# Performance work log

Hardware: AMD Instinct MI355X
Metric: run time of the kernel (lower is better)

The kernel has to match this reference:

```python
import jax, jax.numpy as jnp
import numpy as np

B, S, E, H, O = 4, 2048, 1024, 8, 128

def setup_inputs() -> dict:
    key = jax.random.key(0)
    k1, k2, k3, k4, k5 = jax.random.split(key, 5)
    return {
        "x":  jax.random.normal(k1, (B, S, E), dtype=jnp.float32),
        "Wq": jax.random.normal(k2, (H, E, O), dtype=jnp.float32),
        "Wk": jax.random.normal(k3, (E, O), dtype=jnp.float32),
        "Wv": jax.random.normal(k4, (E, O), dtype=jnp.float32),
        "Wo": jax.random.normal(k5, (O * H, E), dtype=jnp.float32),
    }

def reference(x, Wq, Wk, Wv, Wo):
    # self-attention: kv = x; mode='multihead' (no causal mask), attn_mask=None
    Q = jnp.einsum('bse,heo->bhso', x, Wq)        # (B,H,S,O) per-head query proj
    K = x @ Wk                                     # (B,S,O) shared across heads
    V = x @ Wv                                     # (B,S,O)
    scale = 1.0 / jnp.sqrt(jnp.float32(O))
    scores = jnp.einsum('bhqo,bko->bhqk', Q, K) * scale  # (B,H,S,S)
    probs = jax.nn.softmax(scores, axis=-1)
    ctx = jnp.einsum('bhqk,bko->bhqo', probs, V)   # (B,H,S,O)
    ctx = ctx.transpose(0, 2, 1, 3).reshape(B, S, H * O)  # (B,S,H*O)
    return ctx @ Wo                                # (B,S,E)
```

## Files before the change

kernel.cpp:

```cpp
#include <hip/hip_runtime.h>
#include <math.h>


typedef __attribute__((ext_vector_type(8))) short bf16x8;
typedef __attribute__((ext_vector_type(4))) float f32x4;

#define MFMA(a, b, c) __builtin_amdgcn_mfma_f32_16x16x32_bf16((a), (b), (c), 0, 0, 0)
#define GLB(p) ((const __attribute__((address_space(1))) void*)(p))
#define LDS(p) ((__attribute__((address_space(3))) void*)(p))

#if __has_builtin(__builtin_amdgcn_exp2f)
#define EXP2F(x) __builtin_amdgcn_exp2f(x)
#else
#define EXP2F(x) exp2f(x)
#endif

__device__ __forceinline__ short f2bf(float f) {
    union { float f; unsigned u; } v; v.f = f;
    unsigned r = v.u + 0x7fffu + ((v.u >> 16) & 1u);
    return (short)(r >> 16);
}
__device__ __forceinline__ float bf2f(short s) {
    union { unsigned u; float f; } v; v.u = ((unsigned)(unsigned short)s) << 16;
    return v.f;
}


__global__ __launch_bounds__(256) void split_kernel(
    const float* __restrict__ x, short* __restrict__ hi, short* __restrict__ lo, int n) {
    for (int i = blockIdx.x * blockDim.x + threadIdx.x; i < n; i += gridDim.x * blockDim.x) {
        float f = x[i];
        short h = f2bf(f);
        hi[i] = h;
        lo[i] = f2bf(f - bf2f(h));
    }
}

__global__ __launch_bounds__(256) void build_wt(
    const float* __restrict__ Wq, const float* __restrict__ Wk, const float* __restrict__ Wv,
    short* __restrict__ wth, short* __restrict__ wtl) {
    const int total = 1280 * 1024;
    for (int idx = blockIdx.x * blockDim.x + threadIdx.x; idx < total; idx += gridDim.x * blockDim.x) {
        int n = idx >> 10, k = idx & 1023;
        float f;
        if (n < 1024)      f = Wq[((size_t)(n >> 7) * 1024 + k) * 128 + (n & 127)];
        else if (n < 1152) f = Wk[(size_t)k * 128 + (n - 1024)];
        else               f = Wv[(size_t)k * 128 + (n - 1152)];
        short h = f2bf(f);
        wth[idx] = h;
        wtl[idx] = f2bf(f - bf2f(h));
    }
}

__global__ __launch_bounds__(256) void build_wot(
    const float* __restrict__ Wo, short* __restrict__ wot) {
    const int total = 1024 * 1024;
    for (int idx = blockIdx.x * blockDim.x + threadIdx.x; idx < total; idx += gridDim.x * blockDim.x) {
        int e = idx >> 10, k = idx & 1023;
        wot[idx] = f2bf(Wo[(size_t)k * 1024 + e]);
    }
}

template <int MODE>
__global__ __launch_bounds__(256, 4) void gemm_k(
    const short* __restrict__ Ah, const short* __restrict__ Al,
    const short* __restrict__ Bth, const short* __restrict__ Btl,
    short* __restrict__ qh, short* __restrict__ ql,
    short* __restrict__ kh, short* __restrict__ kl,
    short* __restrict__ vt, float* __restrict__ outf) {
    constexpr int K = 1024;
    __shared__ __align__(16) char smem[33792];
    short* As_h = (short*)smem;
    short* Bs_h = (short*)(smem + 8192);
    short* As_l = (short*)(smem + 16384);
    short* Bs_l = (short*)(smem + 24576);
    unsigned* Ep = (unsigned*)smem;

    const int t = threadIdx.x;
    const int m0 = blockIdx.x * 128, n0 = blockIdx.y * 128;
    const int wave = t >> 6, lane = t & 63;
    const int wr = wave >> 1, wc = wave & 1;
    const int quad = lane >> 4, l16 = lane & 15;
    const bool needLo = (MODE == 0) && (blockIdx.y < 9);

    f32x4 acc[4][4];
    for (int i = 0; i < 4; ++i)
        for (int j = 0; j < 4; ++j) acc[i][j] = (f32x4){0.f, 0.f, 0.f, 0.f};

    for (int kb = 0; kb < K / 32; ++kb) {
        __syncthreads();
        for (int i = 0; i < 2; ++i) {
            int slot = (wave * 2 + i) * 64 + lane;
            int row = slot >> 2, ch = slot & 3;
            int ldsoff = (wave * 2 + i) * 512;
            size_t ga = (size_t)(m0 + row) * K + kb * 32 + ch * 8;
            size_t gb = (size_t)(n0 + row) * K + kb * 32 + ch * 8;
            __builtin_amdgcn_global_load_lds(GLB(Ah + ga), LDS(&As_h[ldsoff]), 16, 0, 0);
            __builtin_amdgcn_global_load_lds(GLB(Bth + gb), LDS(&Bs_h[ldsoff]), 16, 0, 0);
            if constexpr (MODE == 0) {
                if (needLo) {
                    __builtin_amdgcn_global_load_lds(GLB(Al + ga), LDS(&As_l[ldsoff]), 16, 0, 0);
                    __builtin_amdgcn_global_load_lds(GLB(Btl + gb), LDS(&Bs_l[ldsoff]), 16, 0, 0);
                }
            }
        }
        __syncthreads();

        bf16x8 a[4], b[4];
        for (int mi = 0; mi < 4; ++mi)
            a[mi] = *(const bf16x8*)&As_h[(wr * 64 + mi * 16 + l16) * 32 + quad * 8];
        for (int ni = 0; ni < 4; ++ni)
            b[ni] = *(const bf16x8*)&Bs_h[(wc * 64 + ni * 16 + l16) * 32 + quad * 8];
        for (int mi = 0; mi < 4; ++mi)
            for (int ni = 0; ni < 4; ++ni)
                acc[mi][ni] = MFMA(a[mi], b[ni], acc[mi][ni]);
        if constexpr (MODE == 0) {
            if (needLo) {
                bf16x8 al[4], bl[4];
                for (int mi = 0; mi < 4; ++mi)
                    al[mi] = *(const bf16x8*)&As_l[(wr * 64 + mi * 16 + l16) * 32 + quad * 8];
                for (int ni = 0; ni < 4; ++ni)
                    bl[ni] = *(const bf16x8*)&Bs_l[(wc * 64 + ni * 16 + l16) * 32 + quad * 8];
                for (int mi = 0; mi < 4; ++mi)
                    for (int ni = 0; ni < 4; ++ni) {
                        acc[mi][ni] = MFMA(a[mi], bl[ni], acc[mi][ni]);
                        acc[mi][ni] = MFMA(al[mi], b[ni], acc[mi][ni]);
                    }
            }
        }
    }

    const float qscale = 0.12753102455195157f;
    for (int p = 0; p < 2; ++p) {
        __syncthreads();
        if (wr == p) {
            for (int mi = 0; mi < 4; ++mi) {
                int rl = mi * 16 + quad * 4;
                for (int ni = 0; ni < 4; ++ni) {
                    int cl = wc * 64 + ni * 16 + l16;
                    for (int r = 0; r < 4; ++r) {
                        float v = acc[mi][ni][r];
                        unsigned pk;
                        if constexpr (MODE == 0) {
                            if (blockIdx.y < 8) v *= qscale;
                            short hv = f2bf(v);
                            short lv = f2bf(v - bf2f(hv));
                            pk = (unsigned)(unsigned short)hv |
                                 ((unsigned)(unsigned short)lv << 16);
                        } else {
                            union { float f; unsigned u; } cv; cv.f = v; pk = cv.u;
                        }
                        Ep[(rl + r) * 132 + cl] = pk;
                    }
                }
            }
        }
        __syncthreads();

        if constexpr (MODE == 1) {
            for (int j = 0; j < 8; ++j) {
                int cid = t + j * 256;
                int row = cid >> 5, c = cid & 31;
                f32x4 val;
                for (int q = 0; q < 4; ++q) {
                    union { unsigned u; float f; } cv;
                    cv.u = Ep[row * 132 + c * 4 + q];
                    val[q] = cv.f;
                }
                int gr = m0 + p * 64 + row;
                *(f32x4*)&outf[(size_t)gr * 1024 + n0 + c * 4] = val;
            }
        } else if (blockIdx.y < 9) {
            for (int j = 0; j < 4; ++j) {
                int cid = t + j * 256;
                int row = cid >> 4, c = cid & 15;
                bf16x8 hv, lv;
                for (int q = 0; q < 8; ++q) {
                    unsigned w = Ep[row * 132 + c * 8 + q];
                    hv[q] = (short)(w & 0xffffu);
                    lv[q] = (short)(w >> 16);
                }
                int gr = m0 + p * 64 + row;
                int bb = gr >> 11, s = gr & 2047;
                if (blockIdx.y < 8) {
                    size_t base = (((size_t)(bb * 8 + (n0 >> 7))) * 2048 + s) * 128 + c * 8;
                    *(bf16x8*)&qh[base] = hv;
                    *(bf16x8*)&ql[base] = lv;
                } else {
                    size_t base = ((size_t)bb * 2048 + s) * 128 + c * 8;
                    *(bf16x8*)&kh[base] = hv;
                    *(bf16x8*)&kl[base] = lv;
                }
            }
        } else {
            for (int j = 0; j < 4; ++j) {
                int cid = t + j * 256;
                int d = cid >> 3, sc = cid & 7;
                bf16x8 hv;
                for (int q = 0; q < 8; ++q) {
                    unsigned w = Ep[(sc * 8 + q) * 132 + d];
                    hv[q] = (short)(w & 0xffffu);
                }
                int gr0 = m0 + p * 64 + sc * 8;
                int bb = gr0 >> 11, s0 = gr0 & 2047;
                *(bf16x8*)&vt[((size_t)bb * 128 + d) * 2048 + s0] = hv;
            }
        }
    }
}

__global__ __launch_bounds__(256, 2) void attn_k(
    const short* __restrict__ qh, const short* __restrict__ ql,
    const short* __restrict__ kh, const short* __restrict__ kl,
    const short* __restrict__ vt, short* __restrict__ ctx) {
    constexpr int S = 2048, D = 128;
    __shared__ short Kh_s[64 * 128];
    __shared__ short Kl_s[64 * 128];
    __shared__ short Vt_s[128 * 64];
    __shared__ short P_s[128 * 72];

    const int bh = blockIdx.y, b = bh >> 3, h = bh & 7;
    const int q0 = blockIdx.x * 128;
    const int t = threadIdx.x, wave = t >> 6, lane = t & 63;
    const int quad = lane >> 4, l16 = lane & 15;
    const int e8 = l16 & 7;

    bf16x8 bones;
    {
        short o = (l16 == 0) ? (short)0x3F80 : (short)0;
        for (int j = 0; j < 8; ++j) bones[j] = o;
    }

    bf16x8 qfh[2][4], qfl[2][4];
    for (int mb = 0; mb < 2; ++mb) {
        size_t qbase = ((size_t)(b * 8 + h) * S + q0 + wave * 32 + mb * 16 + l16) * D + quad * 8;
        for (int c = 0; c < 4; ++c) {
            qfh[mb][c] = *(const bf16x8*)(qh + qbase + c * 32);
            qfl[mb][c] = *(const bf16x8*)(ql + qbase + c * 32);
        }
    }

    float mrow[2][4];
    f32x4 oacc[2][8], lacc[2];
    for (int mb = 0; mb < 2; ++mb) {
        for (int r = 0; r < 4; ++r) mrow[mb][r] = -INFINITY;
        for (int oi = 0; oi < 8; ++oi) oacc[mb][oi] = (f32x4){0.f, 0.f, 0.f, 0.f};
        lacc[mb] = (f32x4){0.f, 0.f, 0.f, 0.f};
    }

    if (((blockIdx.x + (blockIdx.y << 4)) >> 8) & 1) {
        for (int i = 0; i < 13; ++i) __builtin_amdgcn_s_sleep(7);
    }

    for (int kt = 0; kt < S / 64; ++kt) {
        __syncthreads();
        {
            int pch = lane & 15;
            for (int i = 0; i < 4; ++i) {
                int rk = wave * 16 + i * 4 + (lane >> 4);
                int j = pch ^ (rk & 7);
                size_t g = ((size_t)b * S + kt * 64 + rk) * D + j * 8;
                int ldsoff = (wave * 16 + i * 4) * 128;
                __builtin_amdgcn_global_load_lds(GLB(kh + g), LDS(&Kh_s[ldsoff]), 16, 0, 0);
                __builtin_amdgcn_global_load_lds(GLB(kl + g), LDS(&Kl_s[ldsoff]), 16, 0, 0);
            }
        }
        {
            int pch = lane & 7;
            for (int i = 0; i < 4; ++i) {
                int rv = wave * 32 + i * 8 + (lane >> 3);
                int j = pch ^ (rv & 7);
                size_t g = ((size_t)b * D + rv) * S + kt * 64 + j * 8;
                int ldsoff = (wave * 32 + i * 8) * 64;
                __builtin_amdgcn_global_load_lds(GLB(vt + g), LDS(&Vt_s[ldsoff]), 16, 0, 0);
            }
        }
        __syncthreads();

        f32x4 sacc[2][4];
        for (int mb = 0; mb < 2; ++mb)
            for (int ni = 0; ni < 4; ++ni) sacc[mb][ni] = (f32x4){0.f, 0.f, 0.f, 0.f};
        for (int ni = 0; ni < 4; ++ni) {
            for (int c = 0; c < 4; ++c) {
                int off = (ni * 16 + l16) * 128 + ((c * 4 + quad) ^ e8) * 8;
                bf16x8 kbh = *(const bf16x8*)&Kh_s[off];
                bf16x8 kbl = *(const bf16x8*)&Kl_s[off];
                __builtin_amdgcn_s_setprio(1);
                for (int mb = 0; mb < 2; ++mb) {
                    sacc[mb][ni] = MFMA(qfh[mb][c], kbh, sacc[mb][ni]);
                    sacc[mb][ni] = MFMA(qfl[mb][c], kbh, sacc[mb][ni]);
                    sacc[mb][ni] = MFMA(qfh[mb][c], kbl, sacc[mb][ni]);
                }
                __builtin_amdgcn_s_setprio(0);
            }
        }

        for (int mb = 0; mb < 2; ++mb) {
            for (int r = 0; r < 4; ++r) {
                float mx = fmaxf(fmaxf(sacc[mb][0][r], sacc[mb][1][r]),
                                 fmaxf(sacc[mb][2][r], sacc[mb][3][r]));
                for (int off = 8; off; off >>= 1) mx = fmaxf(mx, __shfl_xor(mx, off));
                float mnew = fmaxf(mrow[mb][r], mx);
                float alpha = EXP2F(mrow[mb][r] - mnew);
                mrow[mb][r] = mnew;
                for (int ni = 0; ni < 4; ++ni)
                    sacc[mb][ni][r] = EXP2F(sacc[mb][ni][r] - mnew);
                lacc[mb][r] *= alpha;
                for (int oi = 0; oi < 8; ++oi) oacc[mb][oi][r] *= alpha;
            }
            for (int ni = 0; ni < 4; ++ni)
                for (int r = 0; r < 4; ++r) {
                    union { float f; unsigned u; } cv; cv.f = sacc[mb][ni][r];
                    P_s[(wave * 32 + mb * 16 + quad * 4 + r) * 72 + ni * 16 + l16] =
                        (short)((cv.u + 0x8000u) >> 16);
                }
        }

        for (int c2 = 0; c2 < 2; ++c2) {
            bf16x8 pa[2];
            for (int mb = 0; mb < 2; ++mb) {
                pa[mb] = *(const bf16x8*)&P_s[(wave * 32 + mb * 16 + l16) * 72 + c2 * 32 + quad * 8];
                lacc[mb] = MFMA(pa[mb], bones, lacc[mb]);
            }
            for (int oi = 0; oi < 8; ++oi) {
                int off = (oi * 16 + l16) * 64 + ((c2 * 4 + quad) ^ e8) * 8;
                bf16x8 vb = *(const bf16x8*)&Vt_s[off];
                __builtin_amdgcn_s_setprio(1);
                for (int mb = 0; mb < 2; ++mb)
                    oacc[mb][oi] = MFMA(pa[mb], vb, oacc[mb][oi]);
                __builtin_amdgcn_s_setprio(0);
            }
        }
    }

    for (int mb = 0; mb < 2; ++mb) {
        for (int r = 0; r < 4; ++r) {
            float ls = __shfl(lacc[mb][r], lane & 48);
            float inv = 1.f / ls;
            int s = q0 + wave * 32 + mb * 16 + quad * 4 + r;
            size_t base = ((size_t)b * S + s) * 1024 + h * 128;
            for (int oi = 0; oi < 8; ++oi)
                ctx[base + oi * 16 + l16] = f2bf(oacc[mb][oi][r] * inv);
        }
    }
}


extern "C" void kernel_launch(void* const* d_in, const int* in_sizes, int n_in,
                              void* d_out, int out_size, void* d_ws, size_t ws_size,
                              hipStream_t stream) {
    const float* x  = (const float*)d_in[0];
    const float* Wq = (const float*)d_in[1];
    const float* Wk = (const float*)d_in[2];
    const float* Wv = (const float*)d_in[3];
    const float* Wo = (const float*)d_in[4];
    float* out = (float*)d_out;

    char* p = (char*)d_ws;
    auto alloc = [&](size_t bytes) { char* r = p; p += bytes; return r; };
    short* xh  = (short*)alloc(16777216);
    short* xl  = (short*)alloc(16777216);
    short* wth = (short*)alloc(2621440);
    short* wtl = (short*)alloc(2621440);
    short* wot = (short*)alloc(2097152);
    short* qh  = (short*)alloc(16777216);
    short* ql  = (short*)alloc(16777216);
    short* kh  = (short*)alloc(2097152);
    short* kl  = (short*)alloc(2097152);
    short* vt  = (short*)alloc(2097152);
    short* ctx = (short*)alloc(16777216);

    split_kernel<<<dim3(2048), dim3(256), 0, stream>>>(x, xh, xl, 8192 * 1024);
    build_wt<<<dim3(1280), dim3(256), 0, stream>>>(Wq, Wk, Wv, wth, wtl);
    build_wot<<<dim3(1024), dim3(256), 0, stream>>>(Wo, wot);
    gemm_k<0><<<dim3(64, 10), dim3(256), 0, stream>>>(xh, xl, wth, wtl,
                                                      qh, ql, kh, kl, vt, nullptr);
    attn_k<<<dim3(16, 32), dim3(256), 0, stream>>>(qh, ql, kh, kl, vt, ctx);
    gemm_k<1><<<dim3(64, 8), dim3(256), 0, stream>>>(ctx, nullptr, wot, nullptr,
                                                     nullptr, nullptr, nullptr, nullptr,
                                                     nullptr, out);
}
```

Before: 359.0 us.

## Vectorize input split, tile-transpose weight prep, drop attention stagger sleep

The fp32-to-bf16 hi/lo split of x now loads four floats at a time and stores packed 4-short vectors. The weight transposes for Wq/Wk/Wv and Wo go through a padded 32x32 shared-memory tile, so both reads and writes are coalesced instead of strided gathers. The s_sleep stagger that delayed half the attention blocks is removed. Together these target memory inefficiency in the preprocessing kernels and idle time in attention, though dropping the stagger may change cache or bandwidth contention patterns.

```diff
diff --git a/kernel.cpp b/kernel.cpp
--- a/kernel.cpp
+++ b/kernel.cpp
@@ -4,6 +4,7 @@
 
 typedef __attribute__((ext_vector_type(8))) short bf16x8;
 typedef __attribute__((ext_vector_type(4))) float f32x4;
+typedef __attribute__((ext_vector_type(4))) short s16x4;
 
 #define MFMA(a, b, c) __builtin_amdgcn_mfma_f32_16x16x32_bf16((a), (b), (c), 0, 0, 0)
 #define GLB(p) ((const __attribute__((address_space(1))) void*)(p))
@@ -27,37 +28,73 @@
 
 
 __global__ __launch_bounds__(256) void split_kernel(
-    const float* __restrict__ x, short* __restrict__ hi, short* __restrict__ lo, int n) {
-    for (int i = blockIdx.x * blockDim.x + threadIdx.x; i < n; i += gridDim.x * blockDim.x) {
-        float f = x[i];
-        short h = f2bf(f);
-        hi[i] = h;
-        lo[i] = f2bf(f - bf2f(h));
+    const float* __restrict__ x, short* __restrict__ hi, short* __restrict__ lo, int n4) {
+    for (int i = blockIdx.x * blockDim.x + threadIdx.x; i < n4; i += gridDim.x * blockDim.x) {
+        f32x4 v = *(const f32x4*)&x[(size_t)i * 4];
+        s16x4 h, l;
+        for (int j = 0; j < 4; ++j) {
+            float f = v[j];
+            short hh = f2bf(f);
+            h[j] = hh;
+            l[j] = f2bf(f - bf2f(hh));
+        }
+        *(s16x4*)&hi[(size_t)i * 4] = h;
+        *(s16x4*)&lo[(size_t)i * 4] = l;
     }
 }
 
 __global__ __launch_bounds__(256) void build_wt(
     const float* __restrict__ Wq, const float* __restrict__ Wk, const float* __restrict__ Wv,
     short* __restrict__ wth, short* __restrict__ wtl) {
-    const int total = 1280 * 1024;
-    for (int idx = blockIdx.x * blockDim.x + threadIdx.x; idx < total; idx += gridDim.x * blockDim.x) {
-        int n = idx >> 10, k = idx & 1023;
-        float f;
-        if (n < 1024)      f = Wq[((size_t)(n >> 7) * 1024 + k) * 128 + (n & 127)];
-        else if (n < 1152) f = Wk[(size_t)k * 128 + (n - 1024)];
-        else               f = Wv[(size_t)k * 128 + (n - 1152)];
-        short h = f2bf(f);
-        wth[idx] = h;
-        wtl[idx] = f2bf(f - bf2f(h));
+    __shared__ float tile[32][33];
+    const int m = blockIdx.z;
+    const int k0 = blockIdx.x * 32, o0 = blockIdx.y * 32;
+    const float* src = (m < 8) ? (Wq + (size_t)m * 1024 * 128) : (m == 8 ? Wk : Wv);
+    const int base_n = (m < 8) ? m * 128 : (m == 8 ? 1024 : 1152);
+    const int t = threadIdx.x;
+    {
+        int tx = t & 31, ty = t >> 5;
+        for (int p = 0; p < 4; ++p)
+            tile[ty + p * 8][tx] = src[(size_t)(k0 + ty + p * 8) * 128 + o0 + tx];
+    }
+    __syncthreads();
+    {
+        int kx = (t & 15) * 2, oy = t >> 4;
+        for (int p = 0; p < 2; ++p) {
+            int o = oy + p * 16;
+            float f0 = tile[kx][o], f1 = tile[kx + 1][o];
+            short h0 = f2bf(f0), h1 = f2bf(f1);
+            short l0 = f2bf(f0 - bf2f(h0)), l1 = f2bf(f1 - bf2f(h1));
+            size_t oidx = (size_t)(base_n + o0 + o) * 1024 + k0 + kx;
+            *(unsigned*)&wth[oidx] = (unsigned)(unsigned short)h0 |
+                                     ((unsigned)(unsigned short)h1 << 16);
+            *(unsigned*)&wtl[oidx] = (unsigned)(unsigned short)l0 |
+                                     ((unsigned)(unsigned short)l1 << 16);
+        }
     }
 }
 
 __global__ __launch_bounds__(256) void build_wot(
     const float* __restrict__ Wo, short* __restrict__ wot) {
-    const int total = 1024 * 1024;
-    for (int idx = blockIdx.x * blockDim.x + threadIdx.x; idx < total; idx += gridDim.x * blockDim.x) {
-        int e = idx >> 10, k = idx & 1023;
-        wot[idx] = f2bf(Wo[(size_t)k * 1024 + e]);
+    __shared__ float tile[32][33];
+    const int k0 = blockIdx.x * 32, e0 = blockIdx.y * 32;
+    const int t = threadIdx.x;
+    {
+        int tx = t & 31, ty = t >> 5;
+        for (int p = 0; p < 4; ++p)
+            tile[ty + p * 8][tx] = Wo[(size_t)(k0 + ty + p * 8) * 1024 + e0 + tx];
+    }
+    __syncthreads();
+    {
+        int kx = (t & 15) * 2, ey = t >> 4;
+        for (int p = 0; p < 2; ++p) {
+            int e = ey + p * 16;
+            float f0 = tile[kx][e], f1 = tile[kx + 1][e];
+            short h0 = f2bf(f0), h1 = f2bf(f1);
+            size_t oidx = (size_t)(e0 + e) * 1024 + k0 + kx;
+            *(unsigned*)&wot[oidx] = (unsigned)(unsigned short)h0 |
+                                     ((unsigned)(unsigned short)h1 << 16);
+        }
     }
 }
 
@@ -248,10 +285,6 @@
         lacc[mb] = (f32x4){0.f, 0.f, 0.f, 0.f};
     }
 
-    if (((blockIdx.x + (blockIdx.y << 4)) >> 8) & 1) {
-        for (int i = 0; i < 13; ++i) __builtin_amdgcn_s_sleep(7);
-    }
-
     for (int kt = 0; kt < S / 64; ++kt) {
         __syncthreads();
         {
@@ -370,9 +403,9 @@
     short* vt  = (short*)alloc(2097152);
     short* ctx = (short*)alloc(16777216);
 
-    split_kernel<<<dim3(2048), dim3(256), 0, stream>>>(x, xh, xl, 8192 * 1024);
-    build_wt<<<dim3(1280), dim3(256), 0, stream>>>(Wq, Wk, Wv, wth, wtl);
-    build_wot<<<dim3(1024), dim3(256), 0, stream>>>(Wo, wot);
+    split_kernel<<<dim3(2048), dim3(256), 0, stream>>>(x, xh, xl, 8192 * 1024 / 4);
+    build_wt<<<dim3(32, 4, 10), dim3(256), 0, stream>>>(Wq, Wk, Wv, wth, wtl);
+    build_wot<<<dim3(32, 32), dim3(256), 0, stream>>>(Wo, wot);
     gemm_k<0><<<dim3(64, 10), dim3(256), 0, stream>>>(xh, xl, wth, wtl,
                                                       qh, ql, kh, kl, vt, nullptr);
     attn_k<<<dim3(16, 32), dim3(256), 0, stream>>>(qh, ql, kh, kl, vt, ctx);
```

After: 346.0 us. 3.6% less time.
